# Kernel optimization log

Hardware: AMD Instinct MI355X
Metric: run time of the kernel (lower is better)

Reference implementation:

```python
import jax, jax.numpy as jnp
import numpy as np


def setup_inputs() -> dict:
    key = jax.random.key(0)
    ks = jax.random.split(key, 7)
    B, T, IN_F = 16384, 64, 48
    F = 32          # feature_size = len(INTERACTIVE_LIST)
    H = 128         # embedding_hidden_size
    TF, TH = T * F, T * H
    scale1 = 1.0 / np.sqrt(TF)
    scale2 = 1.0 / np.sqrt(TH)
    return {
        "x": jax.random.normal(ks[0], (B, T, IN_F), dtype=jnp.float32),
        "W1": jax.random.normal(ks[1], (TF, TH), dtype=jnp.float32) * scale1,
        "b1": jax.random.normal(ks[2], (TH,), dtype=jnp.float32) * scale1,
        "W2": jax.random.normal(ks[3], (TH, TF), dtype=jnp.float32) * scale2,
        "b2": jax.random.normal(ks[4], (TF,), dtype=jnp.float32) * scale2,
        "weight": jax.random.normal(ks[5], (T, F), dtype=jnp.float32),
        "bias": jax.random.normal(ks[6], (F,), dtype=jnp.float32) * (1.0 / np.sqrt(T)),
        "sample_index": jnp.arange(F, dtype=jnp.int32),
    }


def reference(x, W1, b1, W2, b2, weight, bias, sample_index):
    # x: [B, T, IN_F]; gather interactive feature columns -> [B, T, F]
    B = x.shape[0]
    T, F = weight.shape
    xs = jnp.take(x, sample_index, axis=2)            # [B, T, F]
    # pass_linear=True path: MLP on flattened time*feature vector
    h = jax.nn.relu(xs.reshape(B, T * F) @ W1 + b1)   # [B, T*H]; dropout = identity (eval)
    out = (h @ W2 + b2).reshape(B, T, F)              # [B, T, F]
    # vectorized form of the per-sample loop: sum over time of elementwise mul
    emb = jnp.einsum("btf,tf->bf", out, weight) + bias  # [B, F]
    return emb
```

## Files before the change

### kernel.cpp

```cpp
#include <hip/hip_runtime.h>
#include <hip/hip_bf16.h>

#define BATCH 16384
#define TT    64
#define INF   48
#define FF    32
#define TFD   2048
#define THD   8192

typedef __attribute__((ext_vector_type(8))) short bf16x8;
typedef __attribute__((ext_vector_type(4))) short bf16x4;
typedef __attribute__((ext_vector_type(4))) short short4v;
typedef __attribute__((ext_vector_type(4))) float f32x4;

__device__ inline void gload_lds16(const void* g, void* l) {
  __builtin_amdgcn_global_load_lds((const __attribute__((address_space(1))) void*)g,
                                   (__attribute__((address_space(3))) void*)l, 16, 0, 0);
}

__device__ inline f32x4 mfma16x16x16_bf16(bf16x4 a, bf16x4 b, f32x4 c) {
#if __has_builtin(__builtin_amdgcn_mfma_f32_16x16x16bf16_1k)
  return __builtin_amdgcn_mfma_f32_16x16x16bf16_1k(a, b, c, 0, 0, 0);
#else
  asm("v_mfma_f32_16x16x16_bf16 %0, %1, %2, %0" : "+v"(c) : "v"(a), "v"(b));
  return c;
#endif
}

__device__ inline short f32_to_bf16_bits(float x) {
  __hip_bfloat16 h = __float2bfloat16(x);
  return *reinterpret_cast<short*>(&h);
}


__global__ void gather_cast_frag(const float* __restrict__ x, const int* __restrict__ sidx,
                                 __hip_bfloat16* __restrict__ xsf) {
  __shared__ int sx[FF];
  if (threadIdx.x < FF) sx[threadIdx.x] = sidx[threadIdx.x];
  __syncthreads();
  const int b64 = blockIdx.x >> 2;
  const int tq  = blockIdx.x & 3;
  for (int it = 0; it < 16; ++it) {
    const int slot = (tq * 16 + it) * 256 + threadIdx.x;
    const int t  = slot >> 8;
    const int bi = (slot >> 6) & 3;
    const int l  = slot & 63;
    const int lo = l & 15, hi = l >> 4;
    const int row = b64 * 64 + bi * 16 + lo;
    const float* rp = x + ((size_t)row * TT + t) * INF;
    bf16x8 v;
    #pragma unroll
    for (int j = 0; j < 8; ++j) v[j] = f32_to_bf16_bits(rp[sx[hi * 8 + j]]);
    *(bf16x8*)(xsf + ((size_t)b64 * 16384 + slot) * 8) = v;
  }
}

__global__ void transpose_w1(const float* __restrict__ W1, __hip_bfloat16* __restrict__ W1t) {
  __shared__ float tile[64][65];
  const int k0 = blockIdx.x * 64;
  const int n0 = blockIdx.y * 64;
  const int tx = threadIdx.x & 63, ty = threadIdx.x >> 6;
  for (int r = ty; r < 64; r += 4)
    tile[r][tx] = W1[(size_t)(k0 + r) * THD + n0 + tx];
  __syncthreads();
  const int rn = threadIdx.x >> 4;
  const int kq = (threadIdx.x & 15) * 4;
  for (int rr = rn; rr < 64; rr += 16) {
    short4v v;
    #pragma unroll
    for (int i = 0; i < 4; ++i) v[i] = f32_to_bf16_bits(tile[kq + i][rr]);
    *(short4v*)(W1t + (size_t)(n0 + rr) * TFD + k0 + kq) = v;
  }
}

__global__ void make_w2eff(const float* __restrict__ W2, const float* __restrict__ b2,
                           const float* __restrict__ weight, const float* __restrict__ bias,
                           __hip_bfloat16* __restrict__ w2t, float* __restrict__ beff) {
  const int n = blockIdx.x * 8 + (threadIdx.x >> 5);
  const int f = threadIdx.x & 31;
  const float* wr = W2 + (size_t)n * TFD;
  float s = 0.f;
  #pragma unroll 8
  for (int t = 0; t < TT; ++t) s += wr[t * FF + f] * weight[t * FF + f];
  w2t[(size_t)f * THD + n] = __float2bfloat16(s);
  if (blockIdx.x == 0 && threadIdx.x < FF) {
    float sb = bias[f];
    for (int t = 0; t < TT; ++t) sb += b2[t * FF + f] * weight[t * FF + f];
    beff[f] = sb;
  }
}


__device__ inline void stage_w(char* buf, const __hip_bfloat16* __restrict__ w1t,
                               int n0, int k0, int wid, int l) {
  const int sub = l >> 3;
  const int c   = (l & 7) ^ sub;
  const int h   = c >> 2, kc = c & 3;
  const int r0  = wid * 8 + sub;
  const __hip_bfloat16* gw0 = w1t + (size_t)(n0 + 2 * r0 + h) * TFD + k0 + kc * 8;
  const __hip_bfloat16* gw1 = w1t + (size_t)(n0 + 128 + 2 * r0 + h) * TFD + k0 + kc * 8;
  char* lx = buf + wid * 1024;
  gload_lds16(gw0, lx);
  gload_lds16(gw1, lx + 8192);
}

__device__ __forceinline__ void k_iter(char* lds, int t, int n0,
    const char* __restrict__ xbase, const __hip_bfloat16* __restrict__ w1t,
    f32x4 (&acc)[8][4], bf16x8 (&xfu)[4],
    int wbase, int wid, int l) {
  if (t <= 60) stage_w(lds + ((t + 3) & 3) * 16384, w1t, n0, (t + 3) * 32, wid, l);
  __builtin_amdgcn_sched_barrier(0);
  const char* buf = lds + (t & 3) * 16384;
  bf16x8 w0  = *(const bf16x8*)(buf + wbase);
  bf16x8 w1f = *(const bf16x8*)(buf + wbase + 1024);
  #pragma unroll
  for (int g = 0; g < 4; ++g) {
    bf16x8 nw0, nw1;
    if (g < 3) {
      nw0 = *(const bf16x8*)(buf + wbase + (2 * g + 2) * 1024);
      nw1 = *(const bf16x8*)(buf + wbase + (2 * g + 3) * 1024);
    }
    __builtin_amdgcn_s_setprio(1);
    #pragma unroll
    for (int bi = 0; bi < 4; ++bi)
      acc[2 * g][bi] = __builtin_amdgcn_mfma_f32_16x16x32_bf16(w0, xfu[bi], acc[2 * g][bi], 0, 0, 0);
    #pragma unroll
    for (int bi = 0; bi < 4; ++bi)
      acc[2 * g + 1][bi] = __builtin_amdgcn_mfma_f32_16x16x32_bf16(w1f, xfu[bi], acc[2 * g + 1][bi], 0, 0, 0);
    __builtin_amdgcn_s_setprio(0);
    if (g < 3) { w0 = nw0; w1f = nw1; }
  }
  if (t <= 61) {
    #pragma unroll
    for (int bi = 0; bi < 4; ++bi)
      xfu[bi] = *(const bf16x8*)(xbase + ((t + 2) * 4 + bi) * 1024);
  }
  __builtin_amdgcn_sched_barrier(0);
  if (t <= 60)      asm volatile("s_waitcnt vmcnt(6)" ::: "memory");
  else if (t == 61) asm volatile("s_waitcnt vmcnt(4)" ::: "memory");
  else              asm volatile("s_waitcnt vmcnt(0)" ::: "memory");
  __builtin_amdgcn_sched_barrier(0);
  __builtin_amdgcn_s_barrier();
  __builtin_amdgcn_sched_barrier(0);
}

__global__ __launch_bounds__(512, 2) void gemm_fused(
    const __hip_bfloat16* __restrict__ xsf,
    const __hip_bfloat16* __restrict__ w1t,
    const float* __restrict__ b1,
    const __hip_bfloat16* __restrict__ w2t,
    float* __restrict__ partial)
{
  __shared__ __align__(16) char lds[65536];
  const int tid = threadIdx.x;
  const int wid = tid >> 6, l = tid & 63;
  const int mq = wid >> 2, bq = wid & 3;
  const int lo = l & 15, hi = l >> 4;
  const int rl = lo >> 1;
  const int cofs = (((((lo & 1) << 2) | hi) ^ rl) << 4);
  const int strip = blockIdx.x & 7;
  const int bt = blockIdx.x >> 3;
  const int b0 = bt * 256;

  const int wbase = ((mq << 6) + rl) * 128 + cofs;
  const char* xbase = (const char*)xsf + ((size_t)(bt * 4 + bq) * 16384 + l) * 16;

  f32x4 acc2[2][4];
  #pragma unroll
  for (int fi = 0; fi < 2; ++fi)
    #pragma unroll
    for (int bi = 0; bi < 4; ++bi) { f32x4 z = {0.f,0.f,0.f,0.f}; acc2[fi][bi] = z; }

  for (int s = 0; s < 4; ++s) {
    const int n0 = strip * 1024 + s * 256;

    f32x4 acc[8][4];
    #pragma unroll
    for (int mi = 0; mi < 8; ++mi)
      #pragma unroll
      for (int bi = 0; bi < 4; ++bi) { f32x4 z = {0.f,0.f,0.f,0.f}; acc[mi][bi] = z; }

    bf16x8 xfA[4], xfB[4];
    stage_w(lds, w1t, n0, 0, wid, l);
    __builtin_amdgcn_sched_barrier(0);
    #pragma unroll
    for (int bi = 0; bi < 4; ++bi) xfA[bi] = *(const bf16x8*)(xbase + (0 * 4 + bi) * 1024);
    __builtin_amdgcn_sched_barrier(0);
    stage_w(lds + 16384, w1t, n0, 32, wid, l);
    __builtin_amdgcn_sched_barrier(0);
    #pragma unroll
    for (int bi = 0; bi < 4; ++bi) xfB[bi] = *(const bf16x8*)(xbase + (1 * 4 + bi) * 1024);
    __builtin_amdgcn_sched_barrier(0);
    stage_w(lds + 32768, w1t, n0, 64, wid, l);
    __builtin_amdgcn_sched_barrier(0);
    asm volatile("s_waitcnt vmcnt(8)" ::: "memory");
    __builtin_amdgcn_sched_barrier(0);
    __builtin_amdgcn_s_barrier();
    __builtin_amdgcn_sched_barrier(0);

    for (int tt = 0; tt < 64; tt += 2) {
      k_iter(lds, tt,     n0, xbase, w1t, acc, xfA, wbase, wid, l);
      k_iter(lds, tt + 1, n0, xbase, w1t, acc, xfB, wbase, wid, l);
    }

    #pragma unroll
    for (int mi = 0; mi < 8; ++mi) {
      const int nbase = n0 + (mq << 7) + (mi << 4);
      const float4 b1v = *(const float4*)(b1 + nbase + (hi << 2));
      bf16x4 p[4];
      #pragma unroll
      for (int bi = 0; bi < 4; ++bi) {
        bf16x4 pk;
        #pragma unroll
        for (int j = 0; j < 4; ++j) {
          float v = acc[mi][bi][j] + ((const float*)&b1v)[j];
          v = v > 0.f ? v : 0.f;
          pk[j] = f32_to_bf16_bits(v);
        }
        p[bi] = pk;
      }
      bf16x4 a2[2];
      #pragma unroll
      for (int fi = 0; fi < 2; ++fi)
        a2[fi] = *(const bf16x4*)(w2t + (size_t)(fi * 16 + lo) * THD + nbase + (hi << 2));
      #pragma unroll
      for (int fi = 0; fi < 2; ++fi)
        #pragma unroll
        for (int bi = 0; bi < 4; ++bi)
          acc2[fi][bi] = mfma16x16x16_bf16(a2[fi], p[bi], acc2[fi][bi]);
    }
  }

  float* sm = (float*)lds;
  if (mq == 1) {
    #pragma unroll
    for (int fi = 0; fi < 2; ++fi)
      #pragma unroll
      for (int bi = 0; bi < 4; ++bi)
        *(f32x4*)(sm + ((bq << 6) + (bi << 4) + lo) * 32 + fi * 16 + (hi << 2)) = acc2[fi][bi];
  }
  __syncthreads();
  if (mq == 0) {
    #pragma unroll
    for (int fi = 0; fi < 2; ++fi)
      #pragma unroll
      for (int bi = 0; bi < 4; ++bi) {
        f32x4 other = *(const f32x4*)(sm + ((bq << 6) + (bi << 4) + lo) * 32 + fi * 16 + (hi << 2));
        f32x4 v = acc2[fi][bi] + other;
        *(f32x4*)(partial + ((size_t)strip * BATCH + b0 + (bq << 6) + (bi << 4) + lo) * FF + fi * 16 + (hi << 2)) = v;
      }
  }
}

__global__ void reduce_partial(const float* __restrict__ partial, const float* __restrict__ beff,
                               float* __restrict__ out) {
  const int idx = blockIdx.x * 256 + threadIdx.x;
  float s = beff[idx & 31];
  #pragma unroll
  for (int c = 0; c < 8; ++c) s += partial[(size_t)c * BATCH * FF + idx];
  out[idx] = s;
}


extern "C" void kernel_launch(void* const* d_in, const int* in_sizes, int n_in,
                              void* d_out, int out_size, void* d_ws, size_t ws_size,
                              hipStream_t stream) {
  const float* x      = (const float*)d_in[0];
  const float* W1     = (const float*)d_in[1];
  const float* b1     = (const float*)d_in[2];
  const float* W2     = (const float*)d_in[3];
  const float* b2     = (const float*)d_in[4];
  const float* weight = (const float*)d_in[5];
  const float* bias   = (const float*)d_in[6];
  const int*   sidx   = (const int*)d_in[7];

  char* ws = (char*)d_ws;
  __hip_bfloat16* xsf  = (__hip_bfloat16*)ws;
  __hip_bfloat16* w1t  = (__hip_bfloat16*)(ws + 67108864);
  __hip_bfloat16* w2t  = (__hip_bfloat16*)(ws + 100663296);
  float*          beff = (float*)(ws + 101187584);
  float*          part = (float*)(ws + 101188608);

  hipLaunchKernelGGL(gather_cast_frag, dim3(1024), dim3(256), 0, stream, x, sidx, xsf);
  hipLaunchKernelGGL(transpose_w1, dim3(32, 128), dim3(256), 0, stream, W1, w1t);
  hipLaunchKernelGGL(make_w2eff,   dim3(1024),    dim3(256), 0, stream, W2, b2, weight, bias, w2t, beff);
  hipLaunchKernelGGL(gemm_fused,   dim3(512),     dim3(512), 0, stream, xsf, w1t, b1, w2t, part);
  hipLaunchKernelGGL(reduce_partial, dim3(2048),  dim3(256), 0, stream, part, beff, (float*)d_out);
}
```

Baseline: 617.8 us.

## Split k-iteration into two barrier-separated LDS-read and MFMA phases

Restructures the inner K iteration so each wave loads four weight fragments from LDS up front, before issuing the next stage's global-to-LDS copy. It then runs 16 MFMAs and repeats the pattern for the second half, with extra s_barrier and lgkmcnt(0) waits between phases. The aim is a ping-pong style schedule where waves in the workgroup alternate between memory and MFMA phases rather than interleaving loads inside the MFMA loop. The cost is several extra workgroup barriers per iteration and full LDS waits, which may serialize work.

```diff
diff --git a/kernel.cpp b/kernel.cpp
--- a/kernel.cpp
+++ b/kernel.cpp
@@ -108,28 +108,57 @@
     const char* __restrict__ xbase, const __hip_bfloat16* __restrict__ w1t,
     f32x4 (&acc)[8][4], bf16x8 (&xfu)[4],
     int wbase, int wid, int l) {
+  const char* buf = lds + (t & 3) * 16384;
+
+  bf16x8 wa0 = *(const bf16x8*)(buf + wbase);
+  bf16x8 wa1 = *(const bf16x8*)(buf + wbase + 1024);
+  bf16x8 wa2 = *(const bf16x8*)(buf + wbase + 2048);
+  bf16x8 wa3 = *(const bf16x8*)(buf + wbase + 3072);
   if (t <= 60) stage_w(lds + ((t + 3) & 3) * 16384, w1t, n0, (t + 3) * 32, wid, l);
   __builtin_amdgcn_sched_barrier(0);
-  const char* buf = lds + (t & 3) * 16384;
-  bf16x8 w0  = *(const bf16x8*)(buf + wbase);
-  bf16x8 w1f = *(const bf16x8*)(buf + wbase + 1024);
-  #pragma unroll
-  for (int g = 0; g < 4; ++g) {
-    bf16x8 nw0, nw1;
-    if (g < 3) {
-      nw0 = *(const bf16x8*)(buf + wbase + (2 * g + 2) * 1024);
-      nw1 = *(const bf16x8*)(buf + wbase + (2 * g + 3) * 1024);
-    }
-    __builtin_amdgcn_s_setprio(1);
-    #pragma unroll
-    for (int bi = 0; bi < 4; ++bi)
-      acc[2 * g][bi] = __builtin_amdgcn_mfma_f32_16x16x32_bf16(w0, xfu[bi], acc[2 * g][bi], 0, 0, 0);
-    #pragma unroll
-    for (int bi = 0; bi < 4; ++bi)
-      acc[2 * g + 1][bi] = __builtin_amdgcn_mfma_f32_16x16x32_bf16(w1f, xfu[bi], acc[2 * g + 1][bi], 0, 0, 0);
-    __builtin_amdgcn_s_setprio(0);
-    if (g < 3) { w0 = nw0; w1f = nw1; }
-  }
+  __builtin_amdgcn_s_barrier();
+  asm volatile("s_waitcnt lgkmcnt(0)" ::: "memory");
+  __builtin_amdgcn_sched_barrier(0);
+  __builtin_amdgcn_s_setprio(1);
+  #pragma unroll
+  for (int bi = 0; bi < 4; ++bi)
+    acc[0][bi] = __builtin_amdgcn_mfma_f32_16x16x32_bf16(wa0, xfu[bi], acc[0][bi], 0, 0, 0);
+  #pragma unroll
+  for (int bi = 0; bi < 4; ++bi)
+    acc[1][bi] = __builtin_amdgcn_mfma_f32_16x16x32_bf16(wa1, xfu[bi], acc[1][bi], 0, 0, 0);
+  #pragma unroll
+  for (int bi = 0; bi < 4; ++bi)
+    acc[2][bi] = __builtin_amdgcn_mfma_f32_16x16x32_bf16(wa2, xfu[bi], acc[2][bi], 0, 0, 0);
+  #pragma unroll
+  for (int bi = 0; bi < 4; ++bi)
+    acc[3][bi] = __builtin_amdgcn_mfma_f32_16x16x32_bf16(wa3, xfu[bi], acc[3][bi], 0, 0, 0);
+  __builtin_amdgcn_s_setprio(0);
+  __builtin_amdgcn_sched_barrier(0);
+  __builtin_amdgcn_s_barrier();
+
+  bf16x8 wb0 = *(const bf16x8*)(buf + wbase + 4096);
+  bf16x8 wb1 = *(const bf16x8*)(buf + wbase + 5120);
+  bf16x8 wb2 = *(const bf16x8*)(buf + wbase + 6144);
+  bf16x8 wb3 = *(const bf16x8*)(buf + wbase + 7168);
+  __builtin_amdgcn_sched_barrier(0);
+  __builtin_amdgcn_s_barrier();
+  asm volatile("s_waitcnt lgkmcnt(0)" ::: "memory");
+  __builtin_amdgcn_sched_barrier(0);
+  __builtin_amdgcn_s_setprio(1);
+  #pragma unroll
+  for (int bi = 0; bi < 4; ++bi)
+    acc[4][bi] = __builtin_amdgcn_mfma_f32_16x16x32_bf16(wb0, xfu[bi], acc[4][bi], 0, 0, 0);
+  #pragma unroll
+  for (int bi = 0; bi < 4; ++bi)
+    acc[5][bi] = __builtin_amdgcn_mfma_f32_16x16x32_bf16(wb1, xfu[bi], acc[5][bi], 0, 0, 0);
+  #pragma unroll
+  for (int bi = 0; bi < 4; ++bi)
+    acc[6][bi] = __builtin_amdgcn_mfma_f32_16x16x32_bf16(wb2, xfu[bi], acc[6][bi], 0, 0, 0);
+  #pragma unroll
+  for (int bi = 0; bi < 4; ++bi)
+    acc[7][bi] = __builtin_amdgcn_mfma_f32_16x16x32_bf16(wb3, xfu[bi], acc[7][bi], 0, 0, 0);
+  __builtin_amdgcn_s_setprio(0);
+  __builtin_amdgcn_sched_barrier(0);
   if (t <= 61) {
     #pragma unroll
     for (int bi = 0; bi < 4; ++bi)
```

Result: slower. 649.2 us (+5.1%).
